# Kernel tuning notes

Measured on AMD Instinct MI355X. Metric: run time of the kernel, lower is better.

Reference implementation:

```python
import jax, jax.numpy as jnp
import numpy as np

B, S, H = 2, 1024, 2048
NH, NOPE, ROPE, VD = 16, 128, 64, 128
QKD = NOPE + ROPE  # 192
QLR, KVLR = 1536, 512
EPS = 1e-5


def _ln(x, w):
    # torch F.layer_norm with weight, no bias
    m = jnp.mean(x, axis=-1, keepdims=True)
    v = jnp.mean(jnp.square(x - m), axis=-1, keepdims=True)
    return (x - m) * jax.lax.rsqrt(v + EPS) * w


def _rope(x, cos, sin):
    x1, x2 = jnp.split(x, 2, axis=-1)
    return x * cos + jnp.concatenate((-x2, x1), axis=-1) * sin


def setup_inputs() -> dict:
    key = jax.random.key(0)
    ks = jax.random.split(key, 10)
    sd = 0.02
    return {
        "hidden_states": jax.random.normal(ks[0], (B, S, H), jnp.float32),
        "cos": jax.random.uniform(ks[1], (B, S, ROPE), jnp.float32),
        "sin": jax.random.uniform(ks[2], (B, S, ROPE), jnp.float32),
        "w_qa": jax.random.normal(ks[3], (QLR, H), jnp.float32) * sd,
        "q_a_ln_w": jnp.ones((QLR,), jnp.float32),
        "w_qb": jax.random.normal(ks[4], (NH * QKD, QLR), jnp.float32) * sd,
        "w_kva": jax.random.normal(ks[5], (KVLR + ROPE, H), jnp.float32) * sd,
        "kv_a_ln_w": jnp.ones((KVLR,), jnp.float32),
        "W_UK_T": jax.random.normal(ks[6], (NH, NOPE, KVLR), jnp.float32) * sd,
        "W_UV": jax.random.normal(ks[7], (NH, KVLR, VD), jnp.float32) * sd,
        "w_o": jax.random.normal(ks[8], (H, NH * VD), jnp.float32) * sd,
    }


def reference(hidden_states, cos, sin, w_qa, q_a_ln_w, w_qb, w_kva, kv_a_ln_w,
              W_UK_T, W_UV, w_o):
    b, s, _ = hidden_states.shape
    # fused mlapo: low-rank Q path + LN + RoPE
    qa = _ln(hidden_states @ w_qa.T, q_a_ln_w)            # [b,s,QLR]
    q = (qa @ w_qb.T).reshape(b, s, NH, QKD)              # [b,s,h,192]
    q_nope, q_pe = q[..., :NOPE], q[..., NOPE:]
    q_pe = _rope(q_pe, cos[:, :, None, :], sin[:, :, None, :])
    # KV low-rank path (MQA latent) + LN + RoPE on shared k_pe
    kva = hidden_states @ w_kva.T                          # [b,s,KVLR+ROPE]
    kv_c = _ln(kva[..., :KVLR], kv_a_ln_w)                 # [b,s,KVLR]
    k_pe = _rope(kva[..., KVLR:], cos, sin)                # [b,s,ROPE]
    # absorbed latent attention
    q_lat = jnp.einsum('bshd,hdl->bshl', q_nope, W_UK_T)   # [b,s,h,KVLR]
    scores = (jnp.einsum('bqhl,bkl->bhqk', q_lat, kv_c)
              + jnp.einsum('bqhr,bkr->bhqk', q_pe, k_pe)) * (1.0 / np.sqrt(QKD))
    mask = jnp.tril(jnp.ones((s, s), bool))
    scores = jnp.where(mask, scores, jnp.finfo(scores.dtype).min)
    p = jax.nn.softmax(scores, axis=-1)                    # [b,h,q,k]
    ctx = jnp.einsum('bhqk,bkl->bqhl', p, kv_c)            # [b,s,h,KVLR]
    out = jnp.einsum('bqhl,hlv->bqhv', ctx, W_UV)          # [b,s,h,VD]
    return out.reshape(b, s, NH * VD) @ w_o.T              # [b,s,H]
```

## Files before the change

### kernel.cpp

```cpp
#include <hip/hip_runtime.h>
#include <hip/hip_bf16.h>
#include <math.h>

#define BB 2
#define SS 1024
#define HH 2048
#define NHD 16
#define NOPE 128
#define ROPED 64
#define VDIM 128
#define QKD 192
#define QLR 1536
#define KVLR 512
#define EPSF 1e-5f
#define NCOMB 2176

typedef __bf16 bf16x8 __attribute__((ext_vector_type(8)));
typedef float  f32x4  __attribute__((ext_vector_type(4)));

__device__ __forceinline__ void gload_lds16(const __bf16* g, __bf16* l) {
    __builtin_amdgcn_global_load_lds(
        (const __attribute__((address_space(1))) void*)g,
        (__attribute__((address_space(3))) void*)l, 16, 0, 0);
}

__device__ __forceinline__ void swz2d(int nx, int ny, int& bx, int& by) {
    int T = nx * ny;
    int lin = blockIdx.x + nx * blockIdx.y;
    if ((T & 7) == 0) {
        int q = T >> 3;
        lin = (lin & 7) * q + (lin >> 3);
    }
    bx = lin % nx;
    by = lin / nx;
}

template<int BK>
__device__ __forceinline__ void gemm_core_dbuf(
    const __bf16* __restrict__ Ab, const __bf16* __restrict__ Bb,
    int lda, int ldb, int m0, int n0, int K, __bf16* lds, f32x4 acc[4][4])
{
    constexpr int CH    = BK / 8;
    constexpr int LPT   = CH / 2;
    constexpr int BUFE  = 256 * BK;
    constexpr int BOFF  = 128 * BK;
    constexpr int RSTEP = 2048 / BK;
    const int tid = threadIdx.x;
    const int w = tid >> 6, lane = tid & 63, quad = lane >> 4, ln = lane & 15;
    const int wm = (w >> 1) * 64, wn = (w & 1) * 64;
    const int nt = K / BK;

    const int sr  = tid / CH;
    const int spc = tid % CH;
    const int sc  = (BK == 64) ? (spc ^ (sr & 7)) : (spc ^ ((sr >> 1) & 3));
    const __bf16* gA = Ab + (size_t)(m0 + sr) * lda + sc * 8;
    const __bf16* gB = Bb + (size_t)(n0 + sr) * ldb + sc * 8;

    const int swm = (BK == 64) ? ((wm + ln) & 7) : (((wm + ln) >> 1) & 3);
    const int swn = (BK == 64) ? ((wn + ln) & 7) : (((wn + ln) >> 1) & 3);

    auto stage = [&](int buf, int kk) {
        __bf16* la = lds + buf * BUFE + w * 512;
        __bf16* lb = la + BOFF;
        const __bf16* ga = gA + kk;
        const __bf16* gb = gB + kk;
#pragma unroll
        for (int i = 0; i < LPT; ++i) {
            gload_lds16(ga + (size_t)(i * RSTEP) * lda, la + i * 2048);
            gload_lds16(gb + (size_t)(i * RSTEP) * ldb, lb + i * 2048);
        }
    };
    auto wait_stage = [&]() {
        if constexpr (BK == 64) asm volatile("s_waitcnt vmcnt(8)" ::: "memory");
        else                    asm volatile("s_waitcnt vmcnt(4)" ::: "memory");
    };

    stage(0, 0);
    stage(1, BK);
    wait_stage();
    __builtin_amdgcn_s_barrier();
    __builtin_amdgcn_sched_barrier(0);

    for (int t = 0; t < nt; ++t) {
        const int cur = t & 1;
        const __bf16* bufA = lds + cur * BUFE;
        const __bf16* bufB = bufA + BOFF;
        bf16x8 af[BK / 32][4], bv[BK / 32][4];
#pragma unroll
        for (int ks = 0; ks < BK / 32; ++ks)
#pragma unroll
            for (int i = 0; i < 4; ++i) {
                af[ks][i] = *(const bf16x8*)
                    &bufA[(wm + ln) * BK + i * 16 * BK + (((ks * 4 + quad) ^ swm) << 3)];
                bv[ks][i] = *(const bf16x8*)
                    &bufB[(wn + ln) * BK + i * 16 * BK + (((ks * 4 + quad) ^ swn) << 3)];
            }
        __builtin_amdgcn_s_setprio(1);
#pragma unroll
        for (int ks = 0; ks < BK / 32; ++ks)
#pragma unroll
            for (int mi = 0; mi < 4; ++mi)
#pragma unroll
                for (int ni = 0; ni < 4; ++ni)
                    acc[mi][ni] = __builtin_amdgcn_mfma_f32_16x16x32_bf16(
                        af[ks][mi], bv[ks][ni], acc[mi][ni], 0, 0, 0);
        __builtin_amdgcn_s_setprio(0);
        if (t + 1 < nt) {
            __builtin_amdgcn_sched_barrier(0);
            asm volatile("" ::: "memory");
            __builtin_amdgcn_s_barrier();
            asm volatile("" ::: "memory");
            if (t + 2 < nt) {
                stage(cur, (t + 2) * BK);
                wait_stage();
            } else {
                asm volatile("s_waitcnt vmcnt(0)" ::: "memory");
            }
            __builtin_amdgcn_s_barrier();
            __builtin_amdgcn_sched_barrier(0);
        }
    }
}

template<int BK>
__device__ __forceinline__ void gemm_core_tri(
    const __bf16* __restrict__ Ab, const __bf16* __restrict__ Bb,
    int lda, int ldb, int m0, int n0, int K, __bf16* lds, f32x4 acc[4][4])
{
    constexpr int CH    = BK / 8;
    constexpr int LPT   = CH / 2;
    constexpr int BUFE  = 256 * BK;
    constexpr int BOFF  = 128 * BK;
    constexpr int RSTEP = 2048 / BK;
    const int tid = threadIdx.x;
    const int w = tid >> 6, lane = tid & 63, quad = lane >> 4, ln = lane & 15;
    const int wm = (w >> 1) * 64, wn = (w & 1) * 64;
    const int nt = K / BK;

    const int sr  = tid / CH;
    const int spc = tid % CH;
    const int sc  = (BK == 64) ? (spc ^ (sr & 7)) : (spc ^ ((sr >> 1) & 3));
    const __bf16* gA = Ab + (size_t)(m0 + sr) * lda + sc * 8;
    const __bf16* gB = Bb + (size_t)(n0 + sr) * ldb + sc * 8;

    const int swm = (BK == 64) ? ((wm + ln) & 7) : (((wm + ln) >> 1) & 3);
    const int swn = (BK == 64) ? ((wn + ln) & 7) : (((wn + ln) >> 1) & 3);

    auto stage = [&](__bf16* base, int kk) {
        __bf16* la = base + w * 512;
        __bf16* lb = la + BOFF;
        const __bf16* ga = gA + kk;
        const __bf16* gb = gB + kk;
#pragma unroll
        for (int i = 0; i < LPT; ++i) {
            gload_lds16(ga + (size_t)(i * RSTEP) * lda, la + i * 2048);
            gload_lds16(gb + (size_t)(i * RSTEP) * ldb, lb + i * 2048);
        }
    };

    __bf16* p0 = lds;
    __bf16* p1 = lds + BUFE;
    __bf16* p2 = lds + 2 * BUFE;

    stage(p0, 0);
    stage(p1, BK);
    if constexpr (BK == 64) asm volatile("s_waitcnt vmcnt(8)" ::: "memory");
    else                    asm volatile("s_waitcnt vmcnt(4)" ::: "memory");
    __builtin_amdgcn_s_barrier();
    __builtin_amdgcn_sched_barrier(0);

    for (int t = 0; t < nt; ++t) {
        if (t + 2 < nt) stage(p2, (t + 2) * BK);
        bf16x8 af[BK / 32][4], bv[BK / 32][4];
#pragma unroll
        for (int ks = 0; ks < BK / 32; ++ks)
#pragma unroll
            for (int i = 0; i < 4; ++i) {
                af[ks][i] = *(const bf16x8*)
                    &p0[(wm + ln) * BK + i * 16 * BK + (((ks * 4 + quad) ^ swm) << 3)];
                bv[ks][i] = *(const bf16x8*)
                    &p0[BOFF + (wn + ln) * BK + i * 16 * BK + (((ks * 4 + quad) ^ swn) << 3)];
            }
        __builtin_amdgcn_s_setprio(1);
#pragma unroll
        for (int ks = 0; ks < BK / 32; ++ks)
#pragma unroll
            for (int mi = 0; mi < 4; ++mi)
#pragma unroll
                for (int ni = 0; ni < 4; ++ni)
                    acc[mi][ni] = __builtin_amdgcn_mfma_f32_16x16x32_bf16(
                        af[ks][mi], bv[ks][ni], acc[mi][ni], 0, 0, 0);
        __builtin_amdgcn_s_setprio(0);
        if (t + 1 < nt) {
            __builtin_amdgcn_sched_barrier(0);
            if (t + 2 < nt) {
                if constexpr (BK == 64) asm volatile("s_waitcnt vmcnt(8)" ::: "memory");
                else                    asm volatile("s_waitcnt vmcnt(4)" ::: "memory");
            } else {
                asm volatile("s_waitcnt vmcnt(0)" ::: "memory");
            }
            __builtin_amdgcn_s_barrier();
            __builtin_amdgcn_sched_barrier(0);
        }
        __bf16* tmp = p0; p0 = p1; p1 = p2; p2 = tmp;
    }
}

template<bool OUT_BF16, int BK, int MINW, bool TRI>
__global__ __launch_bounds__(256, MINW) void gemm_mfma(
    const __bf16* __restrict__ A, const __bf16* __restrict__ B, void* __restrict__ Cv,
    int M, int N, int K, int lda, int ldb, int ldc,
    long long sA, long long sB, long long sC)
{
    __shared__ __bf16 lds[TRI ? 768 * BK : 512 * BK];
    const __bf16* Ab = A + (long long)blockIdx.z * sA;
    const __bf16* Bb = B + (long long)blockIdx.z * sB;
    const int tid = threadIdx.x;
    const int w = tid >> 6, lane = tid & 63, quad = lane >> 4, ln = lane & 15;
    int bx, by; swz2d(gridDim.x, gridDim.y, bx, by);
    const int m0 = by * 128, n0 = bx * 128;
    const int wm = (w >> 1) * 64, wn = (w & 1) * 64;

    f32x4 acc[4][4];
#pragma unroll
    for (int i = 0; i < 4; ++i)
#pragma unroll
        for (int j = 0; j < 4; ++j) acc[i][j] = (f32x4){0.f, 0.f, 0.f, 0.f};

    if (TRI) gemm_core_tri<BK>(Ab, Bb, lda, ldb, m0, n0, K, lds, acc);
    else     gemm_core_dbuf<BK>(Ab, Bb, lda, ldb, m0, n0, K, lds, acc);

    if (OUT_BF16) {
        __bf16* Cb = (__bf16*)Cv + (long long)blockIdx.z * sC;
#pragma unroll
        for (int mi = 0; mi < 4; ++mi)
#pragma unroll
            for (int r = 0; r < 4; ++r) {
                size_t row = (size_t)(m0 + wm + mi * 16 + quad * 4 + r);
#pragma unroll
                for (int ni = 0; ni < 4; ++ni)
                    Cb[row * ldc + (n0 + wn + ni * 16 + ln)] = (__bf16)acc[mi][ni][r];
            }
    } else {
        float* Cb = (float*)Cv + (long long)blockIdx.z * sC;
#pragma unroll
        for (int mi = 0; mi < 4; ++mi)
#pragma unroll
            for (int r = 0; r < 4; ++r) {
                size_t row = (size_t)(m0 + wm + mi * 16 + quad * 4 + r);
#pragma unroll
                for (int ni = 0; ni < 4; ++ni)
                    Cb[row * ldc + (n0 + wn + ni * 16 + ln)] = acc[mi][ni][r];
            }
    }
}

__global__ __launch_bounds__(256, 3) void gemm_vhkh(
    const __bf16* __restrict__ Wvb, const __bf16* __restrict__ Wuk,
    const __bf16* __restrict__ Kc, __bf16* __restrict__ Vh,
    __bf16* __restrict__ Khb)
{
    int lin = blockIdx.x + 16 * blockIdx.z;
    lin = (lin & 7) * 64 + (lin >> 3);
    const int z = lin >> 4;
    const int sub = lin & 15;
    const int b = z >> 4, h = z & 15;

    __shared__ __bf16 lds[768 * 32];
    const int tid = threadIdx.x;
    const int w = tid >> 6, lane = tid & 63, quad = lane >> 4, ln = lane & 15;
    const int wm = (w >> 1) * 64, wn = (w & 1) * 64;

    f32x4 acc[4][4];
#pragma unroll
    for (int i = 0; i < 4; ++i)
#pragma unroll
        for (int j = 0; j < 4; ++j) acc[i][j] = (f32x4){0.f, 0.f, 0.f, 0.f};

    if (sub < 8) {
        const __bf16* Ab = Wvb + (size_t)h * VDIM * KVLR;
        const __bf16* Bb = Kc + (size_t)b * SS * 576;
        const int m0 = 0, n0 = sub * 128;
        gemm_core_tri<32>(Ab, Bb, KVLR, 576, m0, n0, KVLR, lds, acc);
        __bf16* Cb = Vh + (size_t)z * VDIM * SS;
#pragma unroll
        for (int mi = 0; mi < 4; ++mi)
#pragma unroll
            for (int r = 0; r < 4; ++r) {
                int row = m0 + wm + mi * 16 + quad * 4 + r;
#pragma unroll
                for (int ni = 0; ni < 4; ++ni)
                    Cb[(size_t)row * SS + (n0 + wn + ni * 16 + ln)] = (__bf16)acc[mi][ni][r];
            }
    } else {
        const __bf16* Ab = Kc + (size_t)b * SS * 576;
        const __bf16* Bb = Wuk + (size_t)h * NOPE * KVLR;
        const int m0 = (sub - 8) * 128, n0 = 0;
        gemm_core_tri<32>(Ab, Bb, 576, KVLR, m0, n0, KVLR, lds, acc);
        __bf16* Cb = Khb + (size_t)z * SS * QKD;
#pragma unroll
        for (int mi = 0; mi < 4; ++mi)
#pragma unroll
            for (int r = 0; r < 4; ++r) {
                int row = m0 + wm + mi * 16 + quad * 4 + r;
#pragma unroll
                for (int ni = 0; ni < 4; ++ni)
                    Cb[(size_t)row * QKD + (n0 + wn + ni * 16 + ln)] = (__bf16)acc[mi][ni][r];
            }
    }
}

__global__ __launch_bounds__(256, 3) void gemm_scores(
    const __bf16* __restrict__ qb, const __bf16* __restrict__ Khb,
    __bf16* __restrict__ Sc)
{
    int lin = blockIdx.x + 36 * blockIdx.y;
    lin = (lin & 7) * 144 + (lin >> 3);
    const int z = lin / 36;
    const int i = lin - z * 36;
    int mt = (int)((sqrtf(8.f * i + 1.f) - 1.f) * 0.5f);
    if (mt * (mt + 1) / 2 > i) --mt;
    if ((mt + 1) * (mt + 2) / 2 <= i) ++mt;
    const int nt = i - mt * (mt + 1) / 2;

    const int b = z >> 4, h = z & 15;
    __shared__ __bf16 lds[768 * 32];
    const __bf16* Ab = qb + (size_t)b * SS * (NHD * QKD) + (size_t)h * QKD;
    const __bf16* Bb = Khb + (size_t)z * SS * QKD;
    __bf16* Cb = Sc + (size_t)z * SS * SS;
    const int tid = threadIdx.x;
    const int w = tid >> 6, lane = tid & 63, quad = lane >> 4, ln = lane & 15;
    const int m0 = mt * 128, n0 = nt * 128;
    const int wm = (w >> 1) * 64, wn = (w & 1) * 64;

    f32x4 acc[4][4];
#pragma unroll
    for (int i2 = 0; i2 < 4; ++i2)
#pragma unroll
        for (int j = 0; j < 4; ++j) acc[i2][j] = (f32x4){0.f, 0.f, 0.f, 0.f};

    gemm_core_tri<32>(Ab, Bb, NHD * QKD, QKD, m0, n0, QKD, lds, acc);

    const float SCL2 = 0.07216878364870323f * 1.4426950408889634f;
#pragma unroll
    for (int mi = 0; mi < 4; ++mi)
#pragma unroll
        for (int r = 0; r < 4; ++r) {
            int row = m0 + wm + mi * 16 + quad * 4 + r;
#pragma unroll
            for (int ni = 0; ni < 4; ++ni) {
                int col = n0 + wn + ni * 16 + ln;
                float v = acc[mi][ni][r] * SCL2;
                if (col > row) v = -1e30f;
                Cb[(size_t)row * SS + col] = (__bf16)v;
            }
        }
}

__global__ __launch_bounds__(256) void softmax_kernel(__bf16* __restrict__ Sc)
{
    const int z = blockIdx.y;
    const int w = threadIdx.x >> 6, lane = threadIdx.x & 63;
    const int r = blockIdx.x * 4 + w;
    __bf16* row = Sc + (size_t)z * SS * SS + (size_t)r * SS;
    const int ncols = ((r >> 7) + 1) << 7;
    const int i0 = lane * 8, i1 = i0 + 512;
    const bool a0 = i0 < ncols, a1 = i1 < ncols;
    float v[16];
    float lmax = -1e30f;
    if (a0) {
        bf16x8 c = *(const bf16x8*)(row + i0);
#pragma unroll
        for (int j = 0; j < 8; ++j) { v[j] = (float)c[j]; lmax = fmaxf(lmax, v[j]); }
    }
    if (a1) {
        bf16x8 c = *(const bf16x8*)(row + i1);
#pragma unroll
        for (int j = 0; j < 8; ++j) { v[8 + j] = (float)c[j]; lmax = fmaxf(lmax, v[8 + j]); }
    }
#pragma unroll
    for (int off = 1; off < 64; off <<= 1) lmax = fmaxf(lmax, __shfl_xor(lmax, off));
    float lsum = 0.f;
    if (a0) {
#pragma unroll
        for (int j = 0; j < 8; ++j) { v[j] = __builtin_amdgcn_exp2f(v[j] - lmax); lsum += v[j]; }
    }
    if (a1) {
#pragma unroll
        for (int j = 0; j < 8; ++j) { v[8 + j] = __builtin_amdgcn_exp2f(v[8 + j] - lmax); lsum += v[8 + j]; }
    }
#pragma unroll
    for (int off = 1; off < 64; off <<= 1) lsum += __shfl_xor(lsum, off);
    const float inv = 1.f / lsum;
    if (a0) {
        bf16x8 c;
#pragma unroll
        for (int j = 0; j < 8; ++j) c[j] = (__bf16)(v[j] * inv);
        *(bf16x8*)(row + i0) = c;
    }
    if (a1) {
        bf16x8 c;
#pragma unroll
        for (int j = 0; j < 8; ++j) c[j] = (__bf16)(v[8 + j] * inv);
        *(bf16x8*)(row + i1) = c;
    }
}

__global__ __launch_bounds__(256, 3) void gemm_pv(
    const __bf16* __restrict__ Sc, const __bf16* __restrict__ Vh,
    __bf16* __restrict__ ohb)
{
    int lin = blockIdx.x + 8 * blockIdx.y;
    lin = (lin & 7) * 32 + (lin >> 3);
    const int z = lin >> 3;
    const int mt = lin & 7;

    const int b = z >> 4, h = z & 15;
    const int Keff = (mt + 1) * 128;
    __shared__ __bf16 lds[768 * 32];
    const __bf16* Ab = Sc + (size_t)z * SS * SS;
    const __bf16* Bb = Vh + (size_t)z * VDIM * SS;
    const int tid = threadIdx.x;
    const int w = tid >> 6, lane = tid & 63, quad = lane >> 4, ln = lane & 15;
    const int m0 = mt * 128, n0 = 0;
    const int wm = (w >> 1) * 64, wn = (w & 1) * 64;

    f32x4 acc[4][4];
#pragma unroll
    for (int i = 0; i < 4; ++i)
#pragma unroll
        for (int j = 0; j < 4; ++j) acc[i][j] = (f32x4){0.f, 0.f, 0.f, 0.f};

    gemm_core_tri<32>(Ab, Bb, SS, SS, m0, n0, Keff, lds, acc);

#pragma unroll
    for (int mi = 0; mi < 4; ++mi)
#pragma unroll
        for (int r = 0; r < 4; ++r) {
            int row = m0 + wm + mi * 16 + quad * 4 + r;
            __bf16* op = ohb + (size_t)(b * SS + row) * (NHD * VDIM) + h * VDIM;
#pragma unroll
            for (int ni = 0; ni < 4; ++ni)
                op[n0 + wn + ni * 16 + ln] = (__bf16)acc[mi][ni][r];
        }
}

#define N_XB   (2048LL * 2048)
#define N_CMB  ((long long)NCOMB * HH)
#define N_QBB  (3072LL * 1536)
#define N_WKB  ((long long)NHD * NOPE * KVLR)
#define N_WOB  ((long long)HH * HH)
#define TB1 (N_XB)
#define TB2 (TB1 + N_CMB)
#define TB3 (TB2 + N_QBB)
#define TB4 (TB3 + N_WKB)
#define TB5 (TB4 + N_WOB)

__global__ __launch_bounds__(256) void cast_weights(
    const float* __restrict__ hidden, const float* __restrict__ wqa,
    const float* __restrict__ wkva, const float* __restrict__ wqb,
    const float* __restrict__ wuk, const float* __restrict__ wo,
    __bf16* __restrict__ Xb, __bf16* __restrict__ w_cmb,
    __bf16* __restrict__ w_qbb, __bf16* __restrict__ Wkb,
    __bf16* __restrict__ w_ob)
{
    long long idx = ((long long)blockIdx.x * 256 + threadIdx.x) * 4;
    if (idx >= TB5) return;
    const float* src;
    __bf16* dst;
    if (idx < TB1) { src = hidden + idx; dst = Xb + idx; }
    else if (idx < TB2) {
        long long l = idx - TB1;
        int row = (int)(l >> 11), col = (int)(l & 2047);
        dst = w_cmb + l;
        if (row < 1536)      src = wqa + (size_t)row * 2048 + col;
        else if (row < 2112) src = wkva + (size_t)(row - 1536) * 2048 + col;
        else {
            dst[0] = (__bf16)0.f; dst[1] = (__bf16)0.f;
            dst[2] = (__bf16)0.f; dst[3] = (__bf16)0.f;
            return;
        }
    }
    else if (idx < TB3) { long long l = idx - TB2; src = wqb + l; dst = w_qbb + l; }
    else if (idx < TB4) { long long l = idx - TB3; src = wuk + l; dst = Wkb + l; }
    else                { long long l = idx - TB4; src = wo + l;  dst = w_ob + l; }
    float4 v = *(const float4*)src;
    dst[0] = (__bf16)v.x; dst[1] = (__bf16)v.y;
    dst[2] = (__bf16)v.z; dst[3] = (__bf16)v.w;
}

__global__ __launch_bounds__(256) void transpose_cast(const float* __restrict__ in,
                                                      __bf16* __restrict__ out,
                                                      int R, int C)
{
    __shared__ float t[32][33];
    in  += (size_t)blockIdx.z * R * C;
    out += (size_t)blockIdx.z * R * C;
    int c0 = blockIdx.x * 32, r0 = blockIdx.y * 32;
    int tx = threadIdx.x & 31, ty = threadIdx.x >> 5;
#pragma unroll
    for (int i = 0; i < 4; ++i) {
        int r = ty + i * 8;
        t[r][tx] = in[(size_t)(r0 + r) * C + c0 + tx];
    }
    __syncthreads();
#pragma unroll
    for (int i = 0; i < 4; ++i) {
        int rr = ty + i * 8;
        out[(size_t)(c0 + rr) * R + r0 + tx] = (__bf16)t[tx][rr];
    }
}

__global__ __launch_bounds__(256) void ln_kernel(const float* __restrict__ x,
                                                 const float* __restrict__ w,
                                                 __bf16* __restrict__ y, int N, int ldx)
{
    long long row = blockIdx.x;
    const float* xr = x + row * ldx;
    __bf16* yr = y + row * N;
    int tid = threadIdx.x;
    float s = 0.f, ss = 0.f;
    for (int i = tid; i < N; i += 256) { float v = xr[i]; s += v; ss += v * v; }
#pragma unroll
    for (int off = 32; off > 0; off >>= 1) { s += __shfl_down(s, off); ss += __shfl_down(ss, off); }
    __shared__ float rs[4], rss[4];
    __shared__ float smean, sinv;
    int wave = tid >> 6, lane = tid & 63;
    if (lane == 0) { rs[wave] = s; rss[wave] = ss; }
    __syncthreads();
    if (tid == 0) {
        float S = rs[0] + rs[1] + rs[2] + rs[3];
        float Q = rss[0] + rss[1] + rss[2] + rss[3];
        float mean = S / N;
        float var = Q / N - mean * mean;
        smean = mean; sinv = rsqrtf(var + EPSF);
    }
    __syncthreads();
    float mean = smean, inv = sinv;
    for (int i = tid; i < N; i += 256) yr[i] = (__bf16)((xr[i] - mean) * inv * w[i]);
}

__global__ __launch_bounds__(256) void prep_kernel(
    const float* __restrict__ kva, int ld, const float* __restrict__ kvw,
    const float* __restrict__ cosb, const float* __restrict__ sinb,
    __bf16* __restrict__ Kc, __bf16* __restrict__ q,
    __bf16* __restrict__ Khb)
{
    long long row = blockIdx.x;
    const float* kr = kva + row * ld;
    const float* cr = cosb + row * ROPED;
    const float* sr = sinb + row * ROPED;
    int tid = threadIdx.x;
    float v0 = kr[tid], v1 = kr[tid + 256];
    float s = v0 + v1, ss = v0 * v0 + v1 * v1;
#pragma unroll
    for (int off = 32; off > 0; off >>= 1) { s += __shfl_down(s, off); ss += __shfl_down(ss, off); }
    __shared__ float rs[4], rss[4];
    __shared__ float smean, sinv;
    __shared__ float kpe_s[64];
    int wave = tid >> 6, lane = tid & 63;
    if (lane == 0) { rs[wave] = s; rss[wave] = ss; }
    __syncthreads();
    if (tid == 0) {
        float S = rs[0] + rs[1] + rs[2] + rs[3];
        float Q = rss[0] + rss[1] + rss[2] + rss[3];
        float mean = S / KVLR;
        float var = Q / KVLR - mean * mean;
        smean = mean; sinv = rsqrtf(var + EPSF);
    }
    __syncthreads();
    float mean = smean, inv = sinv;
    __bf16* kc = Kc + row * 576;
    kc[tid]       = (__bf16)((v0 - mean) * inv * kvw[tid]);
    kc[tid + 256] = (__bf16)((v1 - mean) * inv * kvw[tid + 256]);
    if (tid < 32) {
        float x1 = kr[KVLR + tid], x2 = kr[KVLR + 32 + tid];
        float r1 = x1 * cr[tid] - x2 * sr[tid];
        float r2 = x2 * cr[32 + tid] + x1 * sr[32 + tid];
        kc[512 + tid]      = (__bf16)r1;
        kc[512 + 32 + tid] = (__bf16)r2;
        kpe_s[tid]      = r1;
        kpe_s[32 + tid] = r2;
    }
    const int bb = (int)(row >> 10), sp = (int)(row & 1023);
    __bf16* qr = q + row * (NHD * QKD);
#pragma unroll
    for (int j = 0; j < 2; ++j) {
        int idx = tid + j * 256;
        int h = idx >> 5, p = idx & 31;
        __bf16* base = qr + h * QKD + NOPE;
        float x1 = (float)base[p], x2 = (float)base[32 + p];
        base[p]      = (__bf16)(x1 * cr[p] - x2 * sr[p]);
        base[32 + p] = (__bf16)(x2 * cr[32 + p] + x1 * sr[32 + p]);
    }
    __syncthreads();
#pragma unroll
    for (int j = 0; j < 4; ++j) {
        int idx = tid + j * 256;
        int h = idx >> 6, c = idx & 63;
        Khb[((size_t)(bb * NHD + h) * SS + sp) * QKD + NOPE + c] = (__bf16)kpe_s[c];
    }
}

extern "C" void kernel_launch(void* const* d_in, const int* in_sizes, int n_in,
                              void* d_out, int out_size, void* d_ws, size_t ws_size,
                              hipStream_t stream)
{
    const float* hidden    = (const float*)d_in[0];
    const float* cosb      = (const float*)d_in[1];
    const float* sinb      = (const float*)d_in[2];
    const float* w_qa      = (const float*)d_in[3];
    const float* q_a_ln_w  = (const float*)d_in[4];
    const float* w_qb      = (const float*)d_in[5];
    const float* w_kva     = (const float*)d_in[6];
    const float* kv_a_ln_w = (const float*)d_in[7];
    const float* W_UK_T    = (const float*)d_in[8];
    const float* W_UV      = (const float*)d_in[9];
    const float* w_o       = (const float*)d_in[10];
    float* out = (float*)d_out;

    const int M = BB * SS;
    float*  qakva = (float*)d_ws;
    __bf16* Xb    = (__bf16*)(qakva + (size_t)M * NCOMB);
    __bf16* qab   = Xb    + (size_t)M * HH;
    __bf16* Sc    = (__bf16*)d_ws;
    __bf16* qb    = Sc    + (size_t)32 * SS * SS;
    __bf16* Kc    = qb    + (size_t)M * NHD * QKD;
    __bf16* Khb   = Kc    + (size_t)M * 576;
    __bf16* Vh    = Khb   + (size_t)32 * SS * QKD;
    __bf16* ohb   = Vh    + (size_t)32 * VDIM * SS;
    __bf16* w_cmb = ohb   + (size_t)M * HH;
    __bf16* w_qbb = w_cmb + (size_t)NCOMB * HH;
    __bf16* Wkb   = w_qbb + (size_t)NHD * QKD * QLR;
    __bf16* Wvb   = Wkb   + (size_t)NHD * NOPE * KVLR;
    __bf16* w_ob  = Wvb   + (size_t)NHD * VDIM * KVLR;

    dim3 blk(256);

    cast_weights<<<dim3((unsigned)(TB5 / 1024)), blk, 0, stream>>>(
        hidden, w_qa, w_kva, w_qb, W_UK_T, w_o,
        Xb, w_cmb, w_qbb, Wkb, w_ob);
    transpose_cast<<<dim3(VDIM / 32, KVLR / 32, NHD), blk, 0, stream>>>(W_UV, Wvb, KVLR, VDIM);

    gemm_mfma<false, 64, 2, false><<<dim3(NCOMB / 128, M / 128, 1), blk, 0, stream>>>(
        Xb, w_cmb, qakva, M, NCOMB, HH, HH, HH, NCOMB, 0, 0, 0);
    ln_kernel<<<dim3(M), blk, 0, stream>>>(qakva, q_a_ln_w, qab, QLR, NCOMB);
    gemm_mfma<true, 64, 2, false><<<dim3(NHD * QKD / 128, M / 128, 1), blk, 0, stream>>>(
        qab, w_qbb, qb, M, NHD * QKD, QLR, QLR, QLR, NHD * QKD, 0, 0, 0);
    prep_kernel<<<dim3(M), blk, 0, stream>>>(qakva + QLR, NCOMB, kv_a_ln_w,
                                             cosb, sinb, Kc, qb, Khb);
    gemm_vhkh<<<dim3(16, 1, 32), blk, 0, stream>>>(Wvb, Wkb, Kc, Vh, Khb);
    gemm_scores<<<dim3(36, 32), blk, 0, stream>>>(qb, Khb, Sc);
    softmax_kernel<<<dim3(SS / 4, 32), blk, 0, stream>>>(Sc);
    gemm_pv<<<dim3(8, 32), blk, 0, stream>>>(Sc, Vh, ohb);
    gemm_mfma<false, 64, 2, false><<<dim3(HH / 128, M / 128, 1), blk, 0, stream>>>(
        ohb, w_ob, out, M, HH, NHD * VDIM, NHD * VDIM, NHD * VDIM, HH, 0, 0, 0);
}
```

Measured before the change: 285.0 us.

## Split-K the fused QA/KVA GEMM and fuse Q RoPE into the QB GEMM epilogue

The first projection GEMM is split along K into two halves using a z-dimension of 2, writing partial sums to two fp32 buffers. The LayerNorm and prep kernels then add the two partials as they read. This is meant to raise occupancy, since the original grid of 17x16 blocks underfills the GPU. Q RoPE moves out of prep_kernel into a new GEMM epilogue that rotates 64-column tiles aligned to the rope section, which removes a read-modify-write pass over q. The cost is extra fp32 partial-buffer traffic, and the workspace placement of part1 has to avoid overlapping other buffers.

```diff
diff --git a/kernel.cpp b/kernel.cpp
--- a/kernel.cpp
+++ b/kernel.cpp
@@ -253,6 +253,52 @@
                     Cb[row * ldc + (n0 + wn + ni * 16 + ln)] = acc[mi][ni][r];
             }
     }
+}
+
+__global__ __launch_bounds__(256, 2) void gemm_qb_rope(
+    const __bf16* __restrict__ qab, const __bf16* __restrict__ w_qbb,
+    const float* __restrict__ cosb, const float* __restrict__ sinb,
+    __bf16* __restrict__ qb)
+{
+    __shared__ __bf16 lds[512 * 64];
+    const int tid = threadIdx.x;
+    const int w = tid >> 6, lane = tid & 63, quad = lane >> 4, ln = lane & 15;
+    int bx, by; swz2d(gridDim.x, gridDim.y, bx, by);
+    const int m0 = by * 128, n0 = bx * 128;
+    const int wm = (w >> 1) * 64, wn = (w & 1) * 64;
+
+    f32x4 acc[4][4];
+#pragma unroll
+    for (int i = 0; i < 4; ++i)
+#pragma unroll
+        for (int j = 0; j < 4; ++j) acc[i][j] = (f32x4){0.f, 0.f, 0.f, 0.f};
+
+    gemm_core_dbuf<64>(qab, w_qbb, QLR, QLR, m0, n0, QLR, lds, acc);
+
+    const int cq = n0 + wn;
+    const bool isrope = (cq % QKD) == NOPE;
+#pragma unroll
+    for (int mi = 0; mi < 4; ++mi)
+#pragma unroll
+        for (int r = 0; r < 4; ++r) {
+            size_t row = (size_t)(m0 + wm + mi * 16 + quad * 4 + r);
+            __bf16* op = qb + row * (NHD * QKD) + cq;
+            if (isrope) {
+                const float* cr = cosb + row * ROPED;
+                const float* sr = sinb + row * ROPED;
+#pragma unroll
+                for (int ni = 0; ni < 2; ++ni) {
+                    int p = ni * 16 + ln;
+                    float x1 = acc[mi][ni][r], x2 = acc[mi][ni + 2][r];
+                    op[p]      = (__bf16)(x1 * cr[p] - x2 * sr[p]);
+                    op[32 + p] = (__bf16)(x2 * cr[32 + p] + x1 * sr[32 + p]);
+                }
+            } else {
+#pragma unroll
+                for (int ni = 0; ni < 4; ++ni)
+                    op[ni * 16 + ln] = (__bf16)acc[mi][ni][r];
+            }
+        }
 }
 
 __global__ __launch_bounds__(256, 3) void gemm_vhkh(
@@ -512,15 +558,19 @@
 }
 
 __global__ __launch_bounds__(256) void ln_kernel(const float* __restrict__ x,
+                                                 const float* __restrict__ x2,
                                                  const float* __restrict__ w,
                                                  __bf16* __restrict__ y, int N, int ldx)
 {
     long long row = blockIdx.x;
-    const float* xr = x + row * ldx;
+    const float* xr  = x  + row * ldx;
+    const float* x2r = x2 + row * ldx;
     __bf16* yr = y + row * N;
     int tid = threadIdx.x;
     float s = 0.f, ss = 0.f;
-    for (int i = tid; i < N; i += 256) { float v = xr[i]; s += v; ss += v * v; }
+    for (int i = tid; i < N; i += 256) {
+        float v = xr[i] + x2r[i]; s += v; ss += v * v;
+    }
 #pragma unroll
     for (int off = 32; off > 0; off >>= 1) { s += __shfl_down(s, off); ss += __shfl_down(ss, off); }
     __shared__ float rs[4], rss[4];
@@ -537,21 +587,23 @@
     }
     __syncthreads();
     float mean = smean, inv = sinv;
-    for (int i = tid; i < N; i += 256) yr[i] = (__bf16)((xr[i] - mean) * inv * w[i]);
+    for (int i = tid; i < N; i += 256)
+        yr[i] = (__bf16)(((xr[i] + x2r[i]) - mean) * inv * w[i]);
 }
 
 __global__ __launch_bounds__(256) void prep_kernel(
-    const float* __restrict__ kva, int ld, const float* __restrict__ kvw,
+    const float* __restrict__ kva, const float* __restrict__ kva2, int ld,
+    const float* __restrict__ kvw,
     const float* __restrict__ cosb, const float* __restrict__ sinb,
-    __bf16* __restrict__ Kc, __bf16* __restrict__ q,
-    __bf16* __restrict__ Khb)
+    __bf16* __restrict__ Kc, __bf16* __restrict__ Khb)
 {
     long long row = blockIdx.x;
-    const float* kr = kva + row * ld;
+    const float* kr  = kva  + row * ld;
+    const float* k2r = kva2 + row * ld;
     const float* cr = cosb + row * ROPED;
     const float* sr = sinb + row * ROPED;
     int tid = threadIdx.x;
-    float v0 = kr[tid], v1 = kr[tid + 256];
+    float v0 = kr[tid] + k2r[tid], v1 = kr[tid + 256] + k2r[tid + 256];
     float s = v0 + v1, ss = v0 * v0 + v1 * v1;
 #pragma unroll
     for (int off = 32; off > 0; off >>= 1) { s += __shfl_down(s, off); ss += __shfl_down(ss, off); }
@@ -574,7 +626,8 @@
     kc[tid]       = (__bf16)((v0 - mean) * inv * kvw[tid]);
     kc[tid + 256] = (__bf16)((v1 - mean) * inv * kvw[tid + 256]);
     if (tid < 32) {
-        float x1 = kr[KVLR + tid], x2 = kr[KVLR + 32 + tid];
+        float x1 = kr[KVLR + tid] + k2r[KVLR + tid];
+        float x2 = kr[KVLR + 32 + tid] + k2r[KVLR + 32 + tid];
         float r1 = x1 * cr[tid] - x2 * sr[tid];
         float r2 = x2 * cr[32 + tid] + x1 * sr[32 + tid];
         kc[512 + tid]      = (__bf16)r1;
@@ -582,18 +635,8 @@
         kpe_s[tid]      = r1;
         kpe_s[32 + tid] = r2;
     }
+    __syncthreads();
     const int bb = (int)(row >> 10), sp = (int)(row & 1023);
-    __bf16* qr = q + row * (NHD * QKD);
-#pragma unroll
-    for (int j = 0; j < 2; ++j) {
-        int idx = tid + j * 256;
-        int h = idx >> 5, p = idx & 31;
-        __bf16* base = qr + h * QKD + NOPE;
-        float x1 = (float)base[p], x2 = (float)base[32 + p];
-        base[p]      = (__bf16)(x1 * cr[p] - x2 * sr[p]);
-        base[32 + p] = (__bf16)(x2 * cr[32 + p] + x1 * sr[32 + p]);
-    }
-    __syncthreads();
 #pragma unroll
     for (int j = 0; j < 4; ++j) {
         int idx = tid + j * 256;
@@ -623,6 +666,7 @@
     float*  qakva = (float*)d_ws;
     __bf16* Xb    = (__bf16*)(qakva + (size_t)M * NCOMB);
     __bf16* qab   = Xb    + (size_t)M * HH;
+    float*  part1 = (float*)(qab + (size_t)M * QLR);
     __bf16* Sc    = (__bf16*)d_ws;
     __bf16* qb    = Sc    + (size_t)32 * SS * SS;
     __bf16* Kc    = qb    + (size_t)M * NHD * QKD;
@@ -642,14 +686,15 @@
         Xb, w_cmb, w_qbb, Wkb, w_ob);
     transpose_cast<<<dim3(VDIM / 32, KVLR / 32, NHD), blk, 0, stream>>>(W_UV, Wvb, KVLR, VDIM);
 
-    gemm_mfma<false, 64, 2, false><<<dim3(NCOMB / 128, M / 128, 1), blk, 0, stream>>>(
-        Xb, w_cmb, qakva, M, NCOMB, HH, HH, HH, NCOMB, 0, 0, 0);
-    ln_kernel<<<dim3(M), blk, 0, stream>>>(qakva, q_a_ln_w, qab, QLR, NCOMB);
-    gemm_mfma<true, 64, 2, false><<<dim3(NHD * QKD / 128, M / 128, 1), blk, 0, stream>>>(
-        qab, w_qbb, qb, M, NHD * QKD, QLR, QLR, QLR, NHD * QKD, 0, 0, 0);
-    prep_kernel<<<dim3(M), blk, 0, stream>>>(qakva + QLR, NCOMB, kv_a_ln_w,
-                                             cosb, sinb, Kc, qb, Khb);
+    gemm_mfma<false, 64, 2, false><<<dim3(NCOMB / 128, M / 128, 2), blk, 0, stream>>>(
+        Xb, w_cmb, qakva, M, NCOMB, 1024, HH, HH, NCOMB,
+        1024, 1024, (long long)(part1 - qakva));
+    ln_kernel<<<dim3(M), blk, 0, stream>>>(qakva, part1, q_a_ln_w, qab, QLR, NCOMB);
+    prep_kernel<<<dim3(M), blk, 0, stream>>>(qakva + QLR, part1 + QLR, NCOMB,
+                                             kv_a_ln_w, cosb, sinb, Kc, Khb);
     gemm_vhkh<<<dim3(16, 1, 32), blk, 0, stream>>>(Wvb, Wkb, Kc, Vh, Khb);
+    gemm_qb_rope<<<dim3(NHD * QKD / 128, M / 128, 1), blk, 0, stream>>>(
+        qab, w_qbb, cosb, sinb, qb);
     gemm_scores<<<dim3(36, 32), blk, 0, stream>>>(qb, Khb, Sc);
     softmax_kernel<<<dim3(SS / 4, 32), blk, 0, stream>>>(Sc);
     gemm_pv<<<dim3(8, 32), blk, 0, stream>>>(Sc, Vh, ohb);
```

Measured after the change: 287.6 us. Within noise of the previous version (+0.9%).
